# Kernel tuning notes

Hardware: AMD Instinct MI355X
Metric: run time of the kernel (lower is better)

## Reference

```python
import jax, jax.numpy as jnp
import numpy as np

N_NODES = 100000
N_EDGES = 1600000
IN_FEAT = 512
HIDDEN = 128
N_CLASSES = 7


def setup_inputs() -> dict:
    key = jax.random.key(0)
    k1, k2, k3, k4 = jax.random.split(key, 4)
    x = jax.random.normal(k1, (N_NODES, IN_FEAT), dtype=jnp.float32)
    edge_index = jax.random.randint(k2, (2, N_EDGES), 0, N_NODES, dtype=jnp.int64)
    # Glorot-ish init for weights
    W1 = jax.random.normal(k3, (IN_FEAT, HIDDEN), dtype=jnp.float32) / np.sqrt(IN_FEAT)
    b1 = jnp.zeros((HIDDEN,), dtype=jnp.float32)
    W2 = jax.random.normal(k4, (HIDDEN, N_CLASSES), dtype=jnp.float32) / np.sqrt(HIDDEN)
    b2 = jnp.zeros((N_CLASSES,), dtype=jnp.float32)
    return {"x": x, "edge_index": edge_index, "W1": W1, "b1": b1, "W2": W2, "b2": b2}


def gcn_conv(x, edge_index, W, b, n_nodes):
    """PyG GCNConv: linear transform, add self-loops, sym-normalized scatter-add."""
    h = x @ W  # [N, out]
    loop = jnp.arange(n_nodes, dtype=edge_index.dtype)
    src = jnp.concatenate([edge_index[0], loop])
    dst = jnp.concatenate([edge_index[1], loop])
    deg = jax.ops.segment_sum(jnp.ones_like(dst, dtype=h.dtype), dst, num_segments=n_nodes)
    dinv = jnp.where(deg > 0, jax.lax.rsqrt(deg), 0.0)
    norm = dinv[src] * dinv[dst]                 # [E+N]
    msg = h[src] * norm[:, None]                 # irregular gather, scale
    out = jax.ops.segment_sum(msg, dst, num_segments=n_nodes)  # scatter-add
    return out + b


def reference(x, edge_index, W1, b1, W2, b2):
    h = gcn_conv(x, edge_index, W1, b1, N_NODES)
    h = jax.nn.relu(h)
    # dropout(p=0.5) is identity in eval mode (training=False)
    out = gcn_conv(h, edge_index, W2, b2, N_NODES)
    return out
```

## Files before the change

### kernel.cpp

```cpp
#include <hip/hip_runtime.h>
#include <hip/hip_bf16.h>
#include <cstdint>

#define N_NODES_C 100000
#define IN_FEAT 512
#define HIDDEN 128
#define N_CLASSES 7

using f16x8 = __attribute__((ext_vector_type(8))) _Float16;
using f32x4 = __attribute__((ext_vector_type(4))) float;

__global__ void k_zero_int(int* __restrict__ p, int n) {
    int i = blockIdx.x * blockDim.x + threadIdx.x;
    if (i < n) p[i] = 0;
}

__global__ void k_count(const int* __restrict__ dst, int* __restrict__ count, int E) {
    int i = blockIdx.x * blockDim.x + threadIdx.x;
    if (i < E) atomicAdd(&count[dst[i]], 1);
}

__global__ __launch_bounds__(256) void k_partsum(const int* __restrict__ count,
                                                 int* __restrict__ partial, int N) {
    int i = blockIdx.x * 256 + threadIdx.x;
    int c = (i < N) ? count[i] : 0;
    #pragma unroll
    for (int off = 32; off >= 1; off >>= 1) c += __shfl_xor(c, off);
    __shared__ int ws[4];
    if ((threadIdx.x & 63) == 0) ws[threadIdx.x >> 6] = c;
    __syncthreads();
    if (threadIdx.x == 0) partial[blockIdx.x] = ws[0] + ws[1] + ws[2] + ws[3];
}

__global__ __launch_bounds__(512) void k_scan_part(const int* __restrict__ partial,
                                                   int* __restrict__ partoff,
                                                   int* __restrict__ rowp, int NB, int N) {
    __shared__ int s[512];
    int t = threadIdx.x;
    int v = (t < NB) ? partial[t] : 0;
    s[t] = v;
    __syncthreads();
    for (int off = 1; off < 512; off <<= 1) {
        int u = (t >= off) ? s[t - off] : 0;
        __syncthreads();
        s[t] += u;
        __syncthreads();
    }
    if (t < NB) partoff[t] = s[t] - v;
    if (t == 511) rowp[N] = s[511];
}

__global__ __launch_bounds__(256) void k_scan_final(const int* __restrict__ count,
                                                    const int* __restrict__ partoff,
                                                    int* __restrict__ rowp,
                                                    int* __restrict__ cursor,
                                                    float* __restrict__ dinv, int N) {
    __shared__ int wsum[4];
    int i = blockIdx.x * 256 + threadIdx.x;
    int lane = threadIdx.x & 63, w = threadIdx.x >> 6;
    int c = (i < N) ? count[i] : 0;
    int x = c;
    #pragma unroll
    for (int off = 1; off < 64; off <<= 1) {
        int v = __shfl_up(x, off);
        if (lane >= off) x += v;
    }
    if (lane == 63) wsum[w] = x;
    __syncthreads();
    int woff = 0;
    #pragma unroll
    for (int k = 0; k < 4; ++k)
        if (k < w) woff += wsum[k];
    int excl = partoff[blockIdx.x] + woff + x - c;
    if (i < N) {
        rowp[i] = excl;
        cursor[i] = excl;
        dinv[i] = rsqrtf((float)(c + 1));
    }
}

__global__ void k_fill(const int* __restrict__ src, const int* __restrict__ dst,
                       int* __restrict__ cursor, int* __restrict__ csr, int E) {
    int i = blockIdx.x * blockDim.x + threadIdx.x;
    if (i < E) {
        int pos = atomicAdd(&cursor[dst[i]], 1);
        csr[pos] = src[i];
    }
}

__global__ __launch_bounds__(256) void k_prep_w1(const float* __restrict__ W1,
                                                 _Float16* __restrict__ W1T) {
    __shared__ _Float16 tile[16][128];
    const int k0 = blockIdx.x * 16;
    const int t = threadIdx.x;
    #pragma unroll
    for (int i = 0; i < 8; ++i) {
        int idx = i * 256 + t;
        int k = idx >> 7, n = idx & 127;
        tile[k][n] = (_Float16)W1[(size_t)(k0 + k) * HIDDEN + n];
    }
    __syncthreads();
    int n = t >> 1, kh = (t & 1) * 8;
    _Float16 tmp[8];
    #pragma unroll
    for (int i = 0; i < 8; ++i) tmp[i] = tile[kh + i][n];
    *(uint4*)&W1T[(size_t)n * IN_FEAT + k0 + kh] = *(const uint4*)tmp;
}

__global__ __launch_bounds__(256) void k_gemm1(const float* __restrict__ A,
                                               const _Float16* __restrict__ BT,
                                               const float* __restrict__ dinv,
                                               float* __restrict__ t1s, int M) {
    const int wid = threadIdx.x >> 6;
    const int lane = threadIdx.x & 63;
    const int row0 = blockIdx.x * 128 + wid * 32;
    const int r = lane & 15;
    const int kb = lane >> 4;

    f32x4 acc[2][8];
    #pragma unroll
    for (int m = 0; m < 2; ++m)
        #pragma unroll
        for (int j = 0; j < 8; ++j) acc[m][j] = (f32x4){0.f, 0.f, 0.f, 0.f};

    for (int ks = 0; ks < IN_FEAT / 32; ++ks) {
        const int kofs = ks * 32 + kb * 8;
        f16x8 a[2];
        #pragma unroll
        for (int m = 0; m < 2; ++m) {
            int ra = row0 + m * 16 + r;
            float4 v0 = make_float4(0.f, 0.f, 0.f, 0.f), v1 = v0;
            if (ra < M) {
                const float* p = &A[(size_t)ra * IN_FEAT + kofs];
                v0 = *(const float4*)p;
                v1 = *(const float4*)(p + 4);
            }
            a[m][0] = (_Float16)v0.x; a[m][1] = (_Float16)v0.y;
            a[m][2] = (_Float16)v0.z; a[m][3] = (_Float16)v0.w;
            a[m][4] = (_Float16)v1.x; a[m][5] = (_Float16)v1.y;
            a[m][6] = (_Float16)v1.z; a[m][7] = (_Float16)v1.w;
        }
        #pragma unroll
        for (int j = 0; j < 8; ++j) {
            f16x8 b = *(const f16x8*)&BT[(size_t)(j * 16 + r) * IN_FEAT + kofs];
            #pragma unroll
            for (int m = 0; m < 2; ++m)
                acc[m][j] = __builtin_amdgcn_mfma_f32_16x16x32_f16(a[m], b, acc[m][j], 0, 0, 0);
        }
    }

    #pragma unroll
    for (int m = 0; m < 2; ++m) {
        #pragma unroll
        for (int i = 0; i < 4; ++i) {
            int rr = row0 + m * 16 + kb * 4 + i;
            if (rr < M) {
                float dd = dinv[rr];
                #pragma unroll
                for (int j = 0; j < 8; ++j)
                    t1s[(size_t)rr * HIDDEN + j * 16 + r] = acc[m][j][i] * dd;
            }
        }
    }
}

__global__ __launch_bounds__(256) void k_agg1(const float* __restrict__ t1s,
                                              const int* __restrict__ csr,
                                              const int* __restrict__ rowp,
                                              const float* __restrict__ dinv,
                                              const float* __restrict__ b1,
                                              const float* __restrict__ W2,
                                              float* __restrict__ t2s, int N) {
    const int node = blockIdx.x * 4 + (threadIdx.x >> 6);
    if (node >= N) return;
    const int lane = threadIdx.x & 63;
    const int beg = rowp[node], end = rowp[node + 1];
    float ax = 0.f, ay = 0.f;
    for (int e = beg; e < end; ++e) {
        int s = csr[e];
        float2 row = *(const float2*)&t1s[(size_t)s * HIDDEN + lane * 2];
        ax += row.x;
        ay += row.y;
    }
    const float dd = dinv[node];
    float2 self = *(const float2*)&t1s[(size_t)node * HIDDEN + lane * 2];
    float2 bb = *(const float2*)&b1[lane * 2];
    float hx = fmaxf(dd * (ax + self.x) + bb.x, 0.f);
    float hy = fmaxf(dd * (ay + self.y) + bb.y, 0.f);
    float acc[N_CLASSES];
    #pragma unroll
    for (int j = 0; j < N_CLASSES; ++j)
        acc[j] = hx * W2[(2 * lane) * N_CLASSES + j] + hy * W2[(2 * lane + 1) * N_CLASSES + j];
    #pragma unroll
    for (int off = 32; off >= 1; off >>= 1)
        #pragma unroll
        for (int j = 0; j < N_CLASSES; ++j) acc[j] += __shfl_xor(acc[j], off);
    if (lane == 0) {
        #pragma unroll
        for (int j = 0; j < N_CLASSES; ++j)
            t2s[(size_t)node * N_CLASSES + j] = acc[j] * dd;
    }
}

__global__ __launch_bounds__(256) void k_agg2(const float* __restrict__ t2s,
                                              const int* __restrict__ csr,
                                              const int* __restrict__ rowp,
                                              const float* __restrict__ dinv,
                                              const float* __restrict__ b2,
                                              float* __restrict__ out, int N) {
    const int node = blockIdx.x * 32 + (threadIdx.x >> 3);
    const int j = threadIdx.x & 7;
    if (node >= N || j >= N_CLASSES) return;
    const int beg = rowp[node], end = rowp[node + 1];
    float acc = 0.f;
    for (int e = beg; e < end; ++e) {
        int s = csr[e];
        acc += t2s[(size_t)s * N_CLASSES + j];
    }
    float dd = dinv[node];
    out[(size_t)node * N_CLASSES + j] =
        dd * (acc + t2s[(size_t)node * N_CLASSES + j]) + b2[j];
}

extern "C" void kernel_launch(void* const* d_in, const int* in_sizes, int n_in,
                              void* d_out, int out_size, void* d_ws, size_t ws_size,
                              hipStream_t stream) {
    const float* x  = (const float*)d_in[0];
    const int*   ei = (const int*)d_in[1];
    const float* W1 = (const float*)d_in[2];
    const float* b1 = (const float*)d_in[3];
    const float* W2 = (const float*)d_in[4];
    const float* b2 = (const float*)d_in[5];
    float* out = (float*)d_out;

    const int N = N_NODES_C;
    const int E = in_sizes[1] / 2;
    const int* src = ei;
    const int* dst = ei + E;
    const int NB = (N + 255) / 256;

    size_t off = 0;
    auto alloc = [&](size_t bytes) {
        void* p = (char*)d_ws + off;
        off += (bytes + 255) & ~(size_t)255;
        return p;
    };
    int*      count   = (int*)alloc((size_t)N * 4);
    int*      rowp    = (int*)alloc((size_t)(N + 1) * 4);
    int*      cursor  = (int*)alloc((size_t)N * 4);
    int*      csr     = (int*)alloc((size_t)E * 4);
    float*    dinv    = (float*)alloc((size_t)N * 4);
    int*      partial = (int*)alloc((size_t)512 * 4);
    int*      partoff = (int*)alloc((size_t)512 * 4);
    _Float16* W1T     = (_Float16*)alloc((size_t)HIDDEN * IN_FEAT * 2);
    float*    t1s     = (float*)alloc((size_t)N * HIDDEN * 4);
    float*    t2s     = (float*)alloc((size_t)N * N_CLASSES * 4);
    (void)ws_size;

    k_zero_int<<<(N + 255) / 256, 256, 0, stream>>>(count, N);
    k_count<<<(E + 255) / 256, 256, 0, stream>>>(dst, count, E);
    k_partsum<<<NB, 256, 0, stream>>>(count, partial, N);
    k_scan_part<<<1, 512, 0, stream>>>(partial, partoff, rowp, NB, N);
    k_scan_final<<<NB, 256, 0, stream>>>(count, partoff, rowp, cursor, dinv, N);
    k_fill<<<(E + 255) / 256, 256, 0, stream>>>(src, dst, cursor, csr, E);
    k_prep_w1<<<IN_FEAT / 16, 256, 0, stream>>>(W1, W1T);
    k_gemm1<<<(N + 127) / 128, 256, 0, stream>>>(x, W1T, dinv, t1s, N);
    k_agg1<<<(N + 3) / 4, 256, 0, stream>>>(t1s, csr, rowp, dinv, b1, W2, t2s, N);
    k_agg2<<<(N + 31) / 32, 256, 0, stream>>>(t2s, csr, rowp, dinv, b2, out, N);
}
```

Before: 726.5 us.

## Store hidden features in fp16, unroll gathers, pad second-layer rows to 8

The first-layer transformed features are now written and gathered as fp16 instead of fp32, which halves the bytes moved by the irregular 1.6M-edge gather in the first aggregation. Both aggregation loops are unrolled so several independent row loads are in flight per iteration. The second-layer intermediate is padded to stride 8 so it can be written with two float4 stores and read aligned. Rounding to fp16 adds some error to the hidden features.

```diff
diff --git a/kernel.cpp b/kernel.cpp
--- a/kernel.cpp
+++ b/kernel.cpp
@@ -6,8 +6,10 @@
 #define IN_FEAT 512
 #define HIDDEN 128
 #define N_CLASSES 7
+#define T2_STRIDE 8
 
 using f16x8 = __attribute__((ext_vector_type(8))) _Float16;
+using f16x2 = __attribute__((ext_vector_type(2))) _Float16;
 using f32x4 = __attribute__((ext_vector_type(4))) float;
 
 __global__ void k_zero_int(int* __restrict__ p, int n) {
@@ -110,7 +112,7 @@
 __global__ __launch_bounds__(256) void k_gemm1(const float* __restrict__ A,
                                                const _Float16* __restrict__ BT,
                                                const float* __restrict__ dinv,
-                                               float* __restrict__ t1s, int M) {
+                                               _Float16* __restrict__ t1h, int M) {
     const int wid = threadIdx.x >> 6;
     const int lane = threadIdx.x & 63;
     const int row0 = blockIdx.x * 128 + wid * 32;
@@ -158,13 +160,13 @@
                 float dd = dinv[rr];
                 #pragma unroll
                 for (int j = 0; j < 8; ++j)
-                    t1s[(size_t)rr * HIDDEN + j * 16 + r] = acc[m][j][i] * dd;
+                    t1h[(size_t)rr * HIDDEN + j * 16 + r] = (_Float16)(acc[m][j][i] * dd);
             }
         }
     }
 }
 
-__global__ __launch_bounds__(256) void k_agg1(const float* __restrict__ t1s,
+__global__ __launch_bounds__(256) void k_agg1(const _Float16* __restrict__ t1h,
                                               const int* __restrict__ csr,
                                               const int* __restrict__ rowp,
                                               const float* __restrict__ dinv,
@@ -176,17 +178,34 @@
     const int lane = threadIdx.x & 63;
     const int beg = rowp[node], end = rowp[node + 1];
     float ax = 0.f, ay = 0.f;
-    for (int e = beg; e < end; ++e) {
+    int e = beg;
+    for (; e + 8 <= end; e += 8) {
+        int s0 = csr[e + 0], s1 = csr[e + 1], s2 = csr[e + 2], s3 = csr[e + 3];
+        int s4 = csr[e + 4], s5 = csr[e + 5], s6 = csr[e + 6], s7 = csr[e + 7];
+        f16x2 v0 = *(const f16x2*)&t1h[(size_t)s0 * HIDDEN + lane * 2];
+        f16x2 v1 = *(const f16x2*)&t1h[(size_t)s1 * HIDDEN + lane * 2];
+        f16x2 v2 = *(const f16x2*)&t1h[(size_t)s2 * HIDDEN + lane * 2];
+        f16x2 v3 = *(const f16x2*)&t1h[(size_t)s3 * HIDDEN + lane * 2];
+        f16x2 v4 = *(const f16x2*)&t1h[(size_t)s4 * HIDDEN + lane * 2];
+        f16x2 v5 = *(const f16x2*)&t1h[(size_t)s5 * HIDDEN + lane * 2];
+        f16x2 v6 = *(const f16x2*)&t1h[(size_t)s6 * HIDDEN + lane * 2];
+        f16x2 v7 = *(const f16x2*)&t1h[(size_t)s7 * HIDDEN + lane * 2];
+        ax += (float)v0.x + (float)v1.x + (float)v2.x + (float)v3.x
+            + (float)v4.x + (float)v5.x + (float)v6.x + (float)v7.x;
+        ay += (float)v0.y + (float)v1.y + (float)v2.y + (float)v3.y
+            + (float)v4.y + (float)v5.y + (float)v6.y + (float)v7.y;
+    }
+    for (; e < end; ++e) {
         int s = csr[e];
-        float2 row = *(const float2*)&t1s[(size_t)s * HIDDEN + lane * 2];
-        ax += row.x;
-        ay += row.y;
+        f16x2 v = *(const f16x2*)&t1h[(size_t)s * HIDDEN + lane * 2];
+        ax += (float)v.x;
+        ay += (float)v.y;
     }
     const float dd = dinv[node];
-    float2 self = *(const float2*)&t1s[(size_t)node * HIDDEN + lane * 2];
+    f16x2 self = *(const f16x2*)&t1h[(size_t)node * HIDDEN + lane * 2];
     float2 bb = *(const float2*)&b1[lane * 2];
-    float hx = fmaxf(dd * (ax + self.x) + bb.x, 0.f);
-    float hy = fmaxf(dd * (ay + self.y) + bb.y, 0.f);
+    float hx = fmaxf(dd * (ax + (float)self.x) + bb.x, 0.f);
+    float hy = fmaxf(dd * (ay + (float)self.y) + bb.y, 0.f);
     float acc[N_CLASSES];
     #pragma unroll
     for (int j = 0; j < N_CLASSES; ++j)
@@ -196,9 +215,9 @@
         #pragma unroll
         for (int j = 0; j < N_CLASSES; ++j) acc[j] += __shfl_xor(acc[j], off);
     if (lane == 0) {
-        #pragma unroll
-        for (int j = 0; j < N_CLASSES; ++j)
-            t2s[(size_t)node * N_CLASSES + j] = acc[j] * dd;
+        float* row = &t2s[(size_t)node * T2_STRIDE];
+        *(float4*)row = make_float4(acc[0] * dd, acc[1] * dd, acc[2] * dd, acc[3] * dd);
+        *(float4*)(row + 4) = make_float4(acc[4] * dd, acc[5] * dd, acc[6] * dd, 0.f);
     }
 }
 
@@ -210,16 +229,25 @@
                                               float* __restrict__ out, int N) {
     const int node = blockIdx.x * 32 + (threadIdx.x >> 3);
     const int j = threadIdx.x & 7;
-    if (node >= N || j >= N_CLASSES) return;
+    if (node >= N) return;
     const int beg = rowp[node], end = rowp[node + 1];
     float acc = 0.f;
-    for (int e = beg; e < end; ++e) {
-        int s = csr[e];
-        acc += t2s[(size_t)s * N_CLASSES + j];
-    }
-    float dd = dinv[node];
-    out[(size_t)node * N_CLASSES + j] =
-        dd * (acc + t2s[(size_t)node * N_CLASSES + j]) + b2[j];
+    int e = beg;
+    for (; e + 4 <= end; e += 4) {
+        int s0 = csr[e + 0], s1 = csr[e + 1], s2 = csr[e + 2], s3 = csr[e + 3];
+        float a0 = t2s[(size_t)s0 * T2_STRIDE + j];
+        float a1 = t2s[(size_t)s1 * T2_STRIDE + j];
+        float a2 = t2s[(size_t)s2 * T2_STRIDE + j];
+        float a3 = t2s[(size_t)s3 * T2_STRIDE + j];
+        acc += (a0 + a1) + (a2 + a3);
+    }
+    for (; e < end; ++e)
+        acc += t2s[(size_t)csr[e] * T2_STRIDE + j];
+    if (j < N_CLASSES) {
+        float dd = dinv[node];
+        out[(size_t)node * N_CLASSES + j] =
+            dd * (acc + t2s[(size_t)node * T2_STRIDE + j]) + b2[j];
+    }
 }
 
 extern "C" void kernel_launch(void* const* d_in, const int* in_sizes, int n_in,
@@ -253,8 +281,8 @@
     int*      partial = (int*)alloc((size_t)512 * 4);
     int*      partoff = (int*)alloc((size_t)512 * 4);
     _Float16* W1T     = (_Float16*)alloc((size_t)HIDDEN * IN_FEAT * 2);
-    float*    t1s     = (float*)alloc((size_t)N * HIDDEN * 4);
-    float*    t2s     = (float*)alloc((size_t)N * N_CLASSES * 4);
+    _Float16* t1h     = (_Float16*)alloc((size_t)N * HIDDEN * 2);
+    float*    t2s     = (float*)alloc((size_t)N * T2_STRIDE * 4);
     (void)ws_size;
 
     k_zero_int<<<(N + 255) / 256, 256, 0, stream>>>(count, N);
@@ -264,7 +292,7 @@
     k_scan_final<<<NB, 256, 0, stream>>>(count, partoff, rowp, cursor, dinv, N);
     k_fill<<<(E + 255) / 256, 256, 0, stream>>>(src, dst, cursor, csr, E);
     k_prep_w1<<<IN_FEAT / 16, 256, 0, stream>>>(W1, W1T);
-    k_gemm1<<<(N + 127) / 128, 256, 0, stream>>>(x, W1T, dinv, t1s, N);
-    k_agg1<<<(N + 3) / 4, 256, 0, stream>>>(t1s, csr, rowp, dinv, b1, W2, t2s, N);
+    k_gemm1<<<(N + 127) / 128, 256, 0, stream>>>(x, W1T, dinv, t1h, N);
+    k_agg1<<<(N + 3) / 4, 256, 0, stream>>>(t1h, csr, rowp, dinv, b1, W2, t2s, N);
     k_agg2<<<(N + 31) / 32, 256, 0, stream>>>(t2s, csr, rowp, dinv, b2, out, N);
 }
```

New measurement: 644.6 us. 1.13x faster.
